# Kernel optimization log

Hardware: AMD Instinct MI355X
Metric: run time of the kernel (lower is better)

Reference implementation:

```python
import jax, jax.numpy as jnp
import numpy as np

BN_EPS = 1e-5


def haar_dwt2(x):
    # pywt.dwt2(img,'haar'/'db1') -> cA,(cH,cV,cD) with Haar filters lo=[1,1]/sqrt2, hi=[1,-1]/sqrt2.
    # cA=(a+b+c+d)/2, cH('da')=(a+b-c-d)/2, cV('ad')=(a-b+c-d)/2, cD=(a-b-c+d)/2
    # where a=x[2i,2j], b=x[2i,2j+1], c=x[2i+1,2j], d=x[2i+1,2j+1].
    B, C, H, W = x.shape
    xr = x.reshape(B, C, H // 2, 2, W // 2, 2)
    a = xr[:, :, :, 0, :, 0]
    b = xr[:, :, :, 0, :, 1]
    c = xr[:, :, :, 1, :, 0]
    d = xr[:, :, :, 1, :, 1]
    ll = (a + b + c + d) * 0.5
    lh = (a + b - c - d) * 0.5
    hl = (a - b + c - d) * 0.5
    hh = (a - b - c + d) * 0.5
    # interleave per input channel: [LL, LH, HL, HH] -> [B, 4C, H/2, W/2]
    return jnp.stack([ll, lh, hl, hh], axis=2).reshape(B, C * 4, H // 2, W // 2)


def conv_transpose2d(x, w, b):
    # torch ConvTranspose2d(k=4, s=2, p=1); w: [Cin, Cout, 4, 4] (torch layout)
    wk = jnp.flip(w, (-2, -1)).transpose(1, 0, 2, 3)  # [Cout, Cin, 4, 4]
    y = jax.lax.conv_general_dilated(
        x, wk, window_strides=(1, 1), padding=((2, 2), (2, 2)),
        lhs_dilation=(2, 2), dimension_numbers=('NCHW', 'OIHW', 'NCHW'))
    return y + b[None, :, None, None]


def bn_relu(x, g, beta, m, v):
    inv = g * jax.lax.rsqrt(v + BN_EPS)
    return jax.nn.relu((x - m[None, :, None, None]) * inv[None, :, None, None]
                       + beta[None, :, None, None])


def setup_inputs() -> dict:
    key = jax.random.key(0)
    ks = jax.random.split(key, 8)
    Cin, emb_dim = 3, 96
    half = emb_dim // 2  # 48
    B, H, W = 16, 256, 256
    x = jax.random.normal(ks[0], (B, Cin, H, W), dtype=jnp.float32)

    def convT_params(k, cin, cout):
        k1, k2 = jax.random.split(k)
        fan = float(cin * 16)
        w = jax.random.normal(k1, (cin, cout, 4, 4), dtype=jnp.float32) / np.sqrt(fan)
        b = jax.random.normal(k2, (cout,), dtype=jnp.float32) * 0.01
        return w, b

    def bn_params(k, c):
        k1, k2, k3 = jax.random.split(k, 3)
        g = 1.0 + 0.1 * jax.random.normal(k1, (c,), dtype=jnp.float32)
        beta = 0.1 * jax.random.normal(k2, (c,), dtype=jnp.float32)
        m = 0.1 * jax.random.normal(k3, (c,), dtype=jnp.float32)
        v = jnp.ones((c,), dtype=jnp.float32)
        return g, beta, m, v

    w1, b1 = convT_params(ks[1], 4 * Cin, half)
    g1, beta1, m1, v1 = bn_params(ks[2], half)
    w2a, b2a = convT_params(ks[3], 16 * Cin, half)
    g2a, beta2a, m2a, v2a = bn_params(ks[4], half)
    w2b, b2b = convT_params(ks[5], half, half)
    g2b, beta2b, m2b, v2b = bn_params(ks[6], half)

    return dict(x=x, w1=w1, b1=b1, g1=g1, beta1=beta1, m1=m1, v1=v1,
                w2a=w2a, b2a=b2a, g2a=g2a, beta2a=beta2a, m2a=m2a, v2a=v2a,
                w2b=w2b, b2b=b2b, g2b=g2b, beta2b=beta2b, m2b=m2b, v2b=v2b)


def reference(x, w1, b1, g1, beta1, m1, v1,
              w2a, b2a, g2a, beta2a, m2a, v2a,
              w2b, b2b, g2b, beta2b, m2b, v2b):
    x_l1 = haar_dwt2(x)                                  # [B, 4Cin, H/2, W/2]
    out = bn_relu(conv_transpose2d(x_l1, w1, b1), g1, beta1, m1, v1)   # [B, half, H, W]
    x_l2 = haar_dwt2(x_l1)                               # [B, 16Cin, H/4, W/4]
    out2 = bn_relu(conv_transpose2d(x_l2, w2a, b2a), g2a, beta2a, m2a, v2a)
    out2 = bn_relu(conv_transpose2d(out2, w2b, b2b), g2b, beta2b, m2b, v2b)  # [B, half, H, W]
    return jnp.concatenate([out, out2], axis=1)          # [B, emb_dim, H, W]
```

## Files before the change

### kernel.cpp

```cpp
#include <hip/hip_runtime.h>

typedef short s16x8 __attribute__((ext_vector_type(8)));
typedef float f32x4 __attribute__((ext_vector_type(4)));
typedef unsigned short u16;

#define BN_EPS 1e-5f

__device__ __forceinline__ u16 f2bf(float f) {
  union { float f; unsigned u; } v; v.f = f;
  unsigned r = (v.u + 0x7fffu + ((v.u >> 16) & 1u)) >> 16;
  return (u16)r;
}

__device__ void setup_one(
    const float* __restrict__ w, const float* __restrict__ bias,
    const float* __restrict__ g, const float* __restrict__ be,
    const float* __restrict__ mu, const float* __restrict__ var,
    u16* __restrict__ Bp, float* __restrict__ bnp,
    int CIN, int CIP, int KSTEPS, int e)
{
  if (e < 48) {
    float iv = g[e] * rsqrtf(var[e] + BN_EPS);
    bnp[e] = iv;
    bnp[48 + e] = (bias[e] - mu[e]) * iv + be[e];
  }
  int total = 4 * KSTEPS * 1536;
  if (e >= total) return;
  int j = e & 7;
  int l = (e >> 3) & 63;
  int nt = (e >> 9) % 3;
  int sp = e / 1536;
  int s = sp % KSTEPS;
  int p = sp / KSTEPS;
  int py = p >> 1, px = p & 1;
  int n = nt * 16 + (l & 15);
  int k = s * 32 + (l >> 4) * 8 + j;
  int tap = k / CIP, ci = k % CIP;
  int kh = 2 * (tap >> 1) + 1 - py;
  int kw = 2 * (tap & 1) + 1 - px;
  float v = (ci < CIN) ? w[((ci * 48 + n) * 4 + kh) * 4 + kw] : 0.f;
  Bp[e] = f2bf(v);
}

__global__ __launch_bounds__(256) void prep_kernel(
    const float* __restrict__ x, u16* __restrict__ xl1, u16* __restrict__ xl2,
    const float* w1, const float* b1, const float* g1, const float* be1,
    const float* m1, const float* v1, u16* Bp1, float* bnp1,
    const float* w2a, const float* b2a, const float* g2a, const float* be2a,
    const float* m2a, const float* v2a, u16* Bp2a, float* bnp2a,
    const float* w2b, const float* b2b, const float* g2b, const float* be2b,
    const float* m2b, const float* v2b, u16* Bp2b, float* bnp2b)
{
  if (blockIdx.x >= 768) {
    int sub = blockIdx.x - 768;
    int which = sub / 144;
    int e = (sub % 144) * 256 + threadIdx.x;
    if (which == 0)      setup_one(w1, b1, g1, be1, m1, v1, Bp1, bnp1, 12, 16, 2, e);
    else if (which == 1) setup_one(w2a, b2a, g2a, be2a, m2a, v2a, Bp2a, bnp2a, 48, 48, 6, e);
    else                 setup_one(w2b, b2b, g2b, be2b, m2b, v2b, Bp2b, bnp2b, 48, 48, 6, e);
    return;
  }
  int idx = blockIdx.x * 256 + threadIdx.x;
  int w4 = idx & 63; int t = idx >> 6;
  int h4 = t & 63; t >>= 6;
  int c = t % 3; int b = t / 3;
  const float* p = x + (((long)(b * 3 + c) * 256 + 4 * h4) * 256 + 4 * w4);
  float4 r0 = *(const float4*)p;
  float4 r1 = *(const float4*)(p + 256);
  float4 r2 = *(const float4*)(p + 512);
  float4 r3 = *(const float4*)(p + 768);
  float rows[4][4] = {{r0.x, r0.y, r0.z, r0.w}, {r1.x, r1.y, r1.z, r1.w},
                      {r2.x, r2.y, r2.z, r2.w}, {r3.x, r3.y, r3.z, r3.w}};
  float sb[4][2][2];
  #pragma unroll
  for (int qy = 0; qy < 2; ++qy)
    #pragma unroll
    for (int qx = 0; qx < 2; ++qx) {
      float a = rows[2 * qy][2 * qx],      bb = rows[2 * qy][2 * qx + 1];
      float cc = rows[2 * qy + 1][2 * qx], dd = rows[2 * qy + 1][2 * qx + 1];
      sb[0][qy][qx] = (a + bb + cc + dd) * 0.5f;
      sb[1][qy][qx] = (a + bb - cc - dd) * 0.5f;
      sb[2][qy][qx] = (a - bb + cc - dd) * 0.5f;
      sb[3][qy][qx] = (a - bb - cc + dd) * 0.5f;
    }
  #pragma unroll
  for (int s = 0; s < 4; ++s)
    #pragma unroll
    for (int qy = 0; qy < 2; ++qy) {
      unsigned pk = (unsigned)f2bf(sb[s][qy][0]) | ((unsigned)f2bf(sb[s][qy][1]) << 16);
      *(unsigned*)&xl1[(((long)(b * 12 + 4 * c + s) * 128) + 2 * h4 + qy) * 128 + 2 * w4] = pk;
    }
  #pragma unroll
  for (int s = 0; s < 4; ++s) {
    float a = sb[s][0][0], bb = sb[s][0][1], cc = sb[s][1][0], dd = sb[s][1][1];
    float o[4] = {(a + bb + cc + dd) * 0.5f, (a + bb - cc - dd) * 0.5f,
                  (a - bb + cc - dd) * 0.5f, (a - bb - cc + dd) * 0.5f};
    #pragma unroll
    for (int s2 = 0; s2 < 4; ++s2)
      xl2[(((long)(b * 48 + (4 * c + s) * 4 + s2) * 64) + h4) * 64 + w4] = f2bf(o[s2]);
  }
}

template<int CIN, int CIP, int HIN, int WIN, bool OBF16>
__global__ __launch_bounds__(256, 4) void convt_mfma(
    const u16* __restrict__ in,
    const u16* __restrict__ Bp,
    const float* __restrict__ bnp,
    void* __restrict__ outv, int outc, int obase)
{
  constexpr int KSTEPS = CIP / 8;
  constexpr int ITX = 34, ITY = 6;
  constexpr int HOUT = 2 * HIN, WOUT = 2 * WIN;
  __shared__ __align__(16) u16 in_lds[ITX * ITY * CIP];
  __shared__ __align__(16) float out_lds[32 * 2 * 64];

  const int tid = threadIdx.x;
  const int n = blockIdx.z;
  const int qY0 = blockIdx.y * 4;
  const int qX0 = blockIdx.x * 32;

  {
    constexpr int NTASK = CIP * ITY * 4;
    for (int t = tid; t < NTASK; t += 256) {
      int seg = t & 3;
      int rowid = t >> 2;
      int ci = rowid / ITY;
      int y = rowid - ci * ITY;
      int ih = qY0 - 1 + y;
      bool rowok = (CIP == CIN || ci < CIN) && ((unsigned)ih < (unsigned)HIN);
      const u16* gsrc = in + (((long)n * CIN + ci) * HIN + ih) * WIN + qX0 + 8 * seg;
      s16x8 v = {0, 0, 0, 0, 0, 0, 0, 0};
      if (rowok) v = *(const s16x8*)gsrc;
      int base_yx = y * ITX;
      #pragma unroll
      for (int j = 0; j < 8; ++j) {
        int xx = 1 + 8 * seg + j;
        int rot = 8 * ((xx >> 2) & 3);
        if (rot >= CIP) rot -= CIP;
        int cr = ci + rot;
        if (cr >= CIP) cr -= CIP;
        in_lds[(base_yx + xx) * CIP + cr] = (u16)v[j];
      }
      if (seg == 0 || seg == 3) {
        int xh = (seg == 0) ? 0 : 33;
        int iwh = qX0 - 1 + xh;
        u16 hv = 0;
        if (rowok && (unsigned)iwh < (unsigned)WIN) hv = gsrc[(seg == 0) ? -1 : 8];
        int rot = 8 * ((xh >> 2) & 3);
        if (rot >= CIP) rot -= CIP;
        int cr = ci + rot;
        if (cr >= CIP) cr -= CIP;
        in_lds[(base_yx + xh) * CIP + cr] = hv;
      }
    }
  }

  const int wid = tid >> 6, lane = tid & 63;
  const int py = wid >> 1, px = wid & 1;
  const int g = lane >> 4, qx = lane & 15;

  const s16x8* bpp = (const s16x8*)Bp + (wid * KSTEPS * 3) * 64 + lane;

  float4 inv4[3], sh4[3];
  #pragma unroll
  for (int nt = 0; nt < 3; ++nt) {
    inv4[nt] = *(const float4*)&bnp[nt * 16 + 4 * g];
    sh4[nt]  = *(const float4*)&bnp[48 + nt * 16 + 4 * g];
  }

  int abase[KSTEPS];
  #pragma unroll
  for (int s = 0; s < KSTEPS; ++s) {
    int k0 = s * 32 + g * 8;
    int tap = k0 / CIP, ci0 = k0 - tap * CIP;
    int ty = tap >> 1, tx = tap & 1;
    int y = 1 + py - ty;
    int xx = qx + 1 + px - tx;
    int rot = 8 * ((xx >> 2) & 3);
    if (rot >= CIP) rot -= CIP;
    int cr = ci0 + rot;
    if (cr >= CIP) cr -= CIP;
    abase[s] = (y * ITX + xx) * CIP + cr;
  }

  __syncthreads();

  for (int mc = 0; mc < 4; ++mc) {
    f32x4 acc[2][3];
    #pragma unroll
    for (int mt = 0; mt < 2; ++mt)
      #pragma unroll
      for (int nt = 0; nt < 3; ++nt)
        acc[mt][nt] = f32x4{0.f, 0.f, 0.f, 0.f};

    #pragma unroll
    for (int s = 0; s < KSTEPS; ++s) {
      s16x8 bf0 = bpp[(s * 3 + 0) * 64];
      s16x8 bf1 = bpp[(s * 3 + 1) * 64];
      s16x8 bf2 = bpp[(s * 3 + 2) * 64];
      #pragma unroll
      for (int mt = 0; mt < 2; ++mt) {
        s16x8 a = *(const s16x8*)&in_lds[abase[s] + (mc * ITX + mt * 16) * CIP];
        acc[mt][0] = __builtin_amdgcn_mfma_f32_16x16x32_bf16(bf0, a, acc[mt][0], 0, 0, 0);
        acc[mt][1] = __builtin_amdgcn_mfma_f32_16x16x32_bf16(bf1, a, acc[mt][1], 0, 0, 0);
        acc[mt][2] = __builtin_amdgcn_mfma_f32_16x16x32_bf16(bf2, a, acc[mt][2], 0, 0, 0);
      }
    }

    #pragma unroll
    for (int sc = 0; sc < 2; ++sc) {
      const int ntlo = (sc == 0) ? 0 : 2;
      const int ntn  = (sc == 0) ? 2 : 1;
      const int coBase = ntlo * 16;
      __syncthreads();
      #pragma unroll
      for (int ntl = 0; ntl < 2; ++ntl) {
        if (ntl < ntn) {
          const int nt = ntlo + ntl;
          #pragma unroll
          for (int mt = 0; mt < 2; ++mt) {
            #pragma unroll
            for (int r = 0; r < 4; ++r) {
              const int co_rel = ntl * 16 + 4 * g + r;
              float iv = ((const float*)&inv4[nt])[r];
              float sv = ((const float*)&sh4[nt])[r];
              float val = fmaxf(acc[mt][nt][r] * iv + sv, 0.f);
              out_lds[(co_rel * 2 + py) * 64 + 2 * (mt * 16 + qx) + px] = val;
            }
          }
        }
      }
      __syncthreads();
      const int nIter = ntn * 2;
      #pragma unroll
      for (int u = 0; u < 4; ++u) {
        if (u < nIter) {
          int e = u * 256 + tid;
          int ow4 = e & 15, row = e >> 4;
          int co_l = coBase + (row >> 1), ohp = row & 1;
          f32x4 vv = *(const f32x4*)&out_lds[row * 64 + 4 * ow4];
          long off = (((long)(n * outc + obase + co_l) * HOUT + 2 * (qY0 + mc) + ohp) * WOUT)
                     + 2 * qX0 + 4 * ow4;
          if (OBF16) {
            unsigned lo = (unsigned)f2bf(vv.x) | ((unsigned)f2bf(vv.y) << 16);
            unsigned hi = (unsigned)f2bf(vv.z) | ((unsigned)f2bf(vv.w) << 16);
            uint2 pk; pk.x = lo; pk.y = hi;
            *(uint2*)((u16*)outv + off) = pk;
          } else {
            __builtin_nontemporal_store(vv, (f32x4*)((float*)outv + off));
          }
        }
      }
    }
  }
}

extern "C" void kernel_launch(void* const* d_in, const int* in_sizes, int n_in,
                              void* d_out, int out_size, void* d_ws, size_t ws_size,
                              hipStream_t stream) {
  const float* x    = (const float*)d_in[0];
  const float* w1   = (const float*)d_in[1];
  const float* b1   = (const float*)d_in[2];
  const float* g1   = (const float*)d_in[3];
  const float* be1  = (const float*)d_in[4];
  const float* m1   = (const float*)d_in[5];
  const float* v1   = (const float*)d_in[6];
  const float* w2a  = (const float*)d_in[7];
  const float* b2a  = (const float*)d_in[8];
  const float* g2a  = (const float*)d_in[9];
  const float* be2a = (const float*)d_in[10];
  const float* m2a  = (const float*)d_in[11];
  const float* v2a  = (const float*)d_in[12];
  const float* w2b  = (const float*)d_in[13];
  const float* b2b  = (const float*)d_in[14];
  const float* g2b  = (const float*)d_in[15];
  const float* be2b = (const float*)d_in[16];
  const float* m2b  = (const float*)d_in[17];
  const float* v2b  = (const float*)d_in[18];

  float* out = (float*)d_out;
  char* ws = (char*)d_ws;
  u16* xl1  = (u16*)ws;
  u16* xl2  = (u16*)(ws + 6291456);
  u16* o2a  = (u16*)(ws + 12582912);
  u16* Bp1  = (u16*)(ws + 37748736);
  u16* Bp2a = (u16*)(ws + 37773312);
  u16* Bp2b = (u16*)(ws + 37847040);
  float* bnp1  = (float*)(ws + 37920768);
  float* bnp2a = (float*)(ws + 37921152);
  float* bnp2b = (float*)(ws + 37921536);

  prep_kernel<<<1200, 256, 0, stream>>>(
      x, xl1, xl2,
      w1, b1, g1, be1, m1, v1, Bp1, bnp1,
      w2a, b2a, g2a, be2a, m2a, v2a, Bp2a, bnp2a,
      w2b, b2b, g2b, be2b, m2b, v2b, Bp2b, bnp2b);

  convt_mfma<48, 48, 64, 64, true><<<dim3(2, 16, 16), 256, 0, stream>>>(
      xl2, Bp2a, bnp2a, o2a, 48, 0);
  convt_mfma<12, 16, 128, 128, false><<<dim3(4, 32, 16), 256, 0, stream>>>(
      xl1, Bp1, bnp1, out, 96, 0);
  convt_mfma<48, 48, 128, 128, false><<<dim3(4, 32, 16), 256, 0, stream>>>(
      o2a, Bp2b, bnp2b, out, 96, 48);
}
```

Measured before the change: 120.0 us.

## Add dedicated conv1 kernel with wider tile and rotated LDS layout

Replaces the generic templated MFMA conv-transpose launch for the first branch with a specialized kernel. It uses a 64-wide input tile, so half as many blocks, and stores all 48 output channels per wave across three N-tiles. Input is staged in LDS with a channel rotation to avoid bank conflicts. The goal is better reuse of input tiles and weights and less per-block overhead, at the cost of more registers and extra syncthreads during the staged output writes.

```diff
diff --git a/kernel.cpp b/kernel.cpp
--- a/kernel.cpp
+++ b/kernel.cpp
@@ -250,6 +250,138 @@
             __builtin_nontemporal_store(vv, (f32x4*)((float*)outv + off));
           }
         }
+      }
+    }
+  }
+}
+
+__global__ __launch_bounds__(256, 4) void conv1_kernel(
+    const u16* __restrict__ in,
+    const u16* __restrict__ Bp,
+    const float* __restrict__ bnp,
+    float* __restrict__ out)
+{
+  constexpr int CIN = 12, CIP = 16, HIN = 128, WIN = 128;
+  constexpr int KSTEPS = 2;
+  constexpr int ITX = 66, ITY = 6;
+  constexpr int HOUT = 256, WOUT = 256;
+  __shared__ __align__(16) u16 in_lds[ITX * ITY * CIP];
+  __shared__ __align__(16) float out_lds[16 * 2 * 128];
+
+  const int tid = threadIdx.x;
+  const int n = blockIdx.z;
+  const int qY0 = blockIdx.y * 4;
+  const int qX0 = blockIdx.x * 64;
+
+  {
+    constexpr int NTASK = CIP * ITY * 8;
+    for (int t = tid; t < NTASK; t += 256) {
+      int seg = t & 7;
+      int rowid = t >> 3;
+      int ci = rowid / ITY;
+      int y = rowid - ci * ITY;
+      int ih = qY0 - 1 + y;
+      bool rowok = (ci < CIN) && ((unsigned)ih < (unsigned)HIN);
+      const u16* gsrc = in + (((long)n * CIN + ci) * HIN + ih) * WIN + qX0 + 8 * seg;
+      s16x8 v = {0, 0, 0, 0, 0, 0, 0, 0};
+      if (rowok) v = *(const s16x8*)gsrc;
+      int base_yx = y * ITX;
+      #pragma unroll
+      for (int j = 0; j < 8; ++j) {
+        int xx = 1 + 8 * seg + j;
+        int rot = 8 * ((xx >> 2) & 1);
+        int cr = ci + rot;
+        if (cr >= CIP) cr -= CIP;
+        in_lds[(base_yx + xx) * CIP + cr] = (u16)v[j];
+      }
+      if (seg == 0 || seg == 7) {
+        int xh = (seg == 0) ? 0 : 65;
+        int iwh = qX0 - 1 + xh;
+        u16 hv = 0;
+        if (rowok && (unsigned)iwh < (unsigned)WIN) hv = gsrc[(seg == 0) ? -1 : 8];
+        int rot = 8 * ((xh >> 2) & 1);
+        int cr = ci + rot;
+        if (cr >= CIP) cr -= CIP;
+        in_lds[(base_yx + xh) * CIP + cr] = hv;
+      }
+    }
+  }
+
+  const int wid = tid >> 6, lane = tid & 63;
+  const int py = wid >> 1, px = wid & 1;
+  const int g = lane >> 4, qx = lane & 15;
+
+  const s16x8* bpp = (const s16x8*)Bp + (wid * KSTEPS * 3) * 64 + lane;
+
+  float4 inv4[3], sh4[3];
+  #pragma unroll
+  for (int nt = 0; nt < 3; ++nt) {
+    inv4[nt] = *(const float4*)&bnp[nt * 16 + 4 * g];
+    sh4[nt]  = *(const float4*)&bnp[48 + nt * 16 + 4 * g];
+  }
+
+  int abase[KSTEPS];
+  #pragma unroll
+  for (int s = 0; s < KSTEPS; ++s) {
+    int k0 = s * 32 + g * 8;
+    int tap = k0 / CIP, ci0 = k0 - tap * CIP;
+    int ty = tap >> 1, tx = tap & 1;
+    int y = 1 + py - ty;
+    int xx = qx + 1 + px - tx;
+    int rot = 8 * ((xx >> 2) & 1);
+    int cr = ci0 + rot;
+    if (cr >= CIP) cr -= CIP;
+    abase[s] = (y * ITX + xx) * CIP + cr;
+  }
+
+  __syncthreads();
+
+  for (int mc = 0; mc < 4; ++mc) {
+    f32x4 acc[4][3];
+    #pragma unroll
+    for (int mt = 0; mt < 4; ++mt)
+      #pragma unroll
+      for (int nt = 0; nt < 3; ++nt)
+        acc[mt][nt] = f32x4{0.f, 0.f, 0.f, 0.f};
+
+    #pragma unroll
+    for (int s = 0; s < KSTEPS; ++s) {
+      s16x8 bf0 = bpp[(s * 3 + 0) * 64];
+      s16x8 bf1 = bpp[(s * 3 + 1) * 64];
+      s16x8 bf2 = bpp[(s * 3 + 2) * 64];
+      #pragma unroll
+      for (int mt = 0; mt < 4; ++mt) {
+        s16x8 a = *(const s16x8*)&in_lds[abase[s] + (mc * ITX + mt * 16) * CIP];
+        acc[mt][0] = __builtin_amdgcn_mfma_f32_16x16x32_bf16(bf0, a, acc[mt][0], 0, 0, 0);
+        acc[mt][1] = __builtin_amdgcn_mfma_f32_16x16x32_bf16(bf1, a, acc[mt][1], 0, 0, 0);
+        acc[mt][2] = __builtin_amdgcn_mfma_f32_16x16x32_bf16(bf2, a, acc[mt][2], 0, 0, 0);
+      }
+    }
+
+    #pragma unroll
+    for (int nt = 0; nt < 3; ++nt) {
+      __syncthreads();
+      #pragma unroll
+      for (int mt = 0; mt < 4; ++mt) {
+        #pragma unroll
+        for (int r = 0; r < 4; ++r) {
+          const int co_rel = 4 * g + r;
+          float iv = ((const float*)&inv4[nt])[r];
+          float sv = ((const float*)&sh4[nt])[r];
+          float val = fmaxf(acc[mt][nt][r] * iv + sv, 0.f);
+          out_lds[(co_rel * 2 + py) * 128 + 2 * (mt * 16 + qx) + px] = val;
+        }
+      }
+      __syncthreads();
+      #pragma unroll
+      for (int u = 0; u < 4; ++u) {
+        int e = u * 256 + tid;
+        int ow4 = e & 31, row = e >> 5;
+        int co_l = nt * 16 + (row >> 1), ohp = row & 1;
+        f32x4 vv = *(const f32x4*)&out_lds[row * 128 + 4 * ow4];
+        long off = (((long)(n * 96 + co_l) * HOUT + 2 * (qY0 + mc) + ohp) * WOUT)
+                   + 2 * qX0 + 4 * ow4;
+        __builtin_nontemporal_store(vv, (f32x4*)(out + off));
       }
     }
   }
@@ -298,8 +430,7 @@
 
   convt_mfma<48, 48, 64, 64, true><<<dim3(2, 16, 16), 256, 0, stream>>>(
       xl2, Bp2a, bnp2a, o2a, 48, 0);
-  convt_mfma<12, 16, 128, 128, false><<<dim3(4, 32, 16), 256, 0, stream>>>(
-      xl1, Bp1, bnp1, out, 96, 0);
+  conv1_kernel<<<dim3(2, 32, 16), 256, 0, stream>>>(xl1, Bp1, bnp1, out);
   convt_mfma<48, 48, 128, 128, false><<<dim3(4, 32, 16), 256, 0, stream>>>(
       o2a, Bp2b, bnp2b, out, 96, 48);
 }
```

Result: slower. 123.6 us (+3.0%).
